# Kernel tuning notes

Hardware: AMD Instinct MI355X
Metric: run time of the kernel (lower is better)

The kernel has to match this reference:

```python
import jax, jax.numpy as jnp
import numpy as np

N = 100000      # nodes
DEG = 16        # in-degree per node -> E = 1.6M edges
F = 16          # data.x feature dim (19 total - 3 pos dims)
P = 3           # pos dim
H = 64          # hidden_dim
R = 8           # num_regions
C = 8           # num_classes


def _xavier(k, shp):
    lim = np.sqrt(6.0 / (shp[0] + shp[1])).astype(np.float32)
    return jax.random.uniform(k, shp, jnp.float32, -lim, lim)


def setup_inputs() -> dict:
    key = jax.random.key(0)
    ks = jax.random.split(key, 16)
    x = jax.random.normal(ks[0], (N, F), jnp.float32)
    pos = jax.random.uniform(ks[1], (N, P), jnp.float32)
    # every node is a target exactly DEG times so scatter-max is fully covered
    src = jax.random.randint(ks[2], (N * DEG,), 0, N, jnp.int32)
    tgt = jnp.repeat(jnp.arange(N, dtype=jnp.int32), DEG)
    edge_index = jnp.stack([src, tgt])
    # ---- CPU quotient-graph construction (mirrors sklearn KMeans + 3-NN) ----
    pos_np = np.asarray(pos)
    rng = np.random.RandomState(0)
    centers = pos_np[rng.choice(N, R, replace=False)].copy()
    for _ in range(10):  # Lloyd iterations
        d = ((pos_np[:, None, :] - centers[None, :, :]) ** 2).sum(-1)
        labels = d.argmin(1)
        for i in range(R):
            m = labels == i
            if m.any():
                centers[i] = pos_np[m].mean(0)
    cd = ((centers[:, None, :] - centers[None, :, :]) ** 2).sum(-1)
    nn_idx = np.argsort(cd, axis=1)[:, :3]
    conn = []
    for i in range(R):
        for j in nn_idx[i, 1:]:
            conn.append([i, j]); conn.append([j, i])
    quotient_edge_index = jnp.asarray(np.array(conn).T, jnp.int32)
    cluster_labels = jnp.asarray(labels, jnp.int32)
    # ---- parameters (xavier_uniform weights, zero bias) ----
    out = dict(x=x, pos=pos, edge_index=edge_index,
               cluster_labels=cluster_labels,
               quotient_edge_index=quotient_edge_index)
    in_dims = [2 * (F + P), 2 * H, 2 * H, 2 * H]
    for i in range(4):
        out[f"conv{i+1}_W1"] = _xavier(ks[3 + 2 * i], (in_dims[i], H))
        out[f"conv{i+1}_b1"] = jnp.zeros((H,), jnp.float32)
        out[f"conv{i+1}_W2"] = _xavier(ks[4 + 2 * i], (H, H))
        out[f"conv{i+1}_b2"] = jnp.zeros((H,), jnp.float32)
    out["lin_W"] = _xavier(ks[11], (H, C))
    out["lin_b"] = jnp.zeros((C,), jnp.float32)
    return out


def _edge_conv(x, edge_index, W1, b1, W2, b2, num_nodes):
    src, tgt = edge_index[0], edge_index[1]
    x_i = x[tgt]                         # [E, d] target (center)
    x_j = x[src]                         # [E, d] source (neighbor)
    m = jnp.concatenate([x_i, x_j - x_i], axis=1)   # [E, 2d]
    m = jax.nn.relu(m @ W1 + b1) @ W2 + b2          # [E, H]
    agg = jax.ops.segment_max(m, tgt, num_segments=num_nodes)
    # nodes with no incoming edges -> 0 (torch_scatter semantics)
    return jnp.where(jnp.isfinite(agg), agg, 0.0)


def reference(x, pos, edge_index, cluster_labels, quotient_edge_index,
              conv1_W1, conv1_b1, conv1_W2, conv1_b2,
              conv2_W1, conv2_b1, conv2_W2, conv2_b2,
              conv3_W1, conv3_b1, conv3_W2, conv3_b2,
              conv4_W1, conv4_b1, conv4_W2, conv4_b2,
              lin_W, lin_b):
    h = jnp.concatenate([x, pos], axis=1)                       # [N, 19]
    h = jax.nn.relu(_edge_conv(h, edge_index, conv1_W1, conv1_b1, conv1_W2, conv1_b2, N))
    h = jax.nn.relu(_edge_conv(h, edge_index, conv2_W1, conv2_b1, conv2_W2, conv2_b2, N))
    # quotient graph: per-region mean of node features
    sums = jax.ops.segment_sum(h, cluster_labels, num_segments=R)        # [R, H]
    cnt = jax.ops.segment_sum(jnp.ones((h.shape[0], 1), h.dtype), cluster_labels, num_segments=R)
    qx = jnp.where(cnt > 0, sums / jnp.maximum(cnt, 1.0), 0.0)           # [R, H]
    qx = jax.nn.relu(_edge_conv(qx, quotient_edge_index, conv3_W1, conv3_b1, conv3_W2, conv3_b2, R))
    qx = jax.nn.relu(_edge_conv(qx, quotient_edge_index, conv4_W1, conv4_b1, conv4_W2, conv4_b2, R))
    graph_emb = qx.sum(axis=0, keepdims=True)                    # global_add_pool -> [1, H]
    return graph_emb @ lin_W + lin_b                             # [1, C]
```

## Files before the change

kernel.cpp:

```cpp
#include <hip/hip_runtime.h>
#include <hip/hip_fp16.h>

typedef float fv4 __attribute__((ext_vector_type(4)));
using hf8   = __attribute__((ext_vector_type(8))) _Float16;
using f32x4 = __attribute__((ext_vector_type(4))) float;
using u32x4 = __attribute__((ext_vector_type(4))) unsigned;
using u32x2 = __attribute__((ext_vector_type(2))) unsigned;

#define HDIM 64
#define QBANKS 64

__device__ __forceinline__ unsigned short f16r(float f) {
    return __half_as_ushort(__float2half(f));
}
__device__ __forceinline__ float hs2f(unsigned short s) {
    return __half2float(__ushort_as_half(s));
}
__device__ __forceinline__ unsigned addrelu2(unsigned ua, unsigned va) {
    unsigned s, r;
    asm("v_pk_add_f16 %0, %1, %2" : "=v"(s) : "v"(ua), "v"(va));
    asm("v_pk_max_f16 %0, %1, 0" : "=v"(r) : "v"(s));
    return r;
}

__global__ void pre1_kernel(
    const float* __restrict__ x, const float* __restrict__ pos,
    const float* __restrict__ W1, const float* __restrict__ b1,
    unsigned short* __restrict__ U, unsigned short* __restrict__ V, int N,
    int mainBlocks,
    const float* __restrict__ W2a, const float* __restrict__ W2b,
    const float* __restrict__ W1c,
    unsigned short* __restrict__ hiA, unsigned short* __restrict__ loA,
    unsigned short* __restrict__ hiB, unsigned short* __restrict__ loB,
    unsigned short* __restrict__ wph, unsigned short* __restrict__ wpl,
    const int* __restrict__ labels, int* __restrict__ qcnt)
{
    if ((int)blockIdx.x >= mainBlocks) {
        int idx = (blockIdx.x - mainBlocks) * 256 + threadIdx.x;
        if (idx < 4096) {
            int j = idx >> 6, c = idx & 63;
            float w = W2a[idx];
            unsigned short h = f16r(w);
            unsigned short l = f16r(w - hs2f(h));
            hiA[c * 64 + j] = h; loA[c * 64 + j] = l;
            w = W2b[idx];
            h = f16r(w);
            l = f16r(w - hs2f(h));
            hiB[c * 64 + j] = h; loB[c * 64 + j] = l;
        }
        if (idx < 8192) {
            int d = idx & 63, cp = idx >> 6;
            float w = (cp < 64) ? (W1c[d * 64 + cp] - W1c[(d + 64) * 64 + cp])
                                : W1c[(d + 64) * 64 + (cp - 64)];
            unsigned short h = f16r(w);
            unsigned short l = f16r(w - hs2f(h));
            wph[cp * 64 + d] = h;
            wpl[cp * 64 + d] = l;
        }
        {
            __shared__ int lh[8];
            int loc[8] = {0, 0, 0, 0, 0, 0, 0, 0};
            for (int n = idx; n < N; n += 8192) {
                int l = labels[n];
#pragma unroll
                for (int r = 0; r < 8; ++r) loc[r] += (l == r) ? 1 : 0;
            }
            if (threadIdx.x < 8) lh[threadIdx.x] = 0;
            __syncthreads();
#pragma unroll
            for (int r = 0; r < 8; ++r) if (loc[r]) atomicAdd(&lh[r], loc[r]);
            __syncthreads();
            if (threadIdx.x < 8) atomicAdd(&qcnt[threadIdx.x], lh[threadIdx.x]);
        }
        return;
    }

    int lane = threadIdx.x & 63;
    int gw   = (blockIdx.x * blockDim.x + threadIdx.x) >> 6;
    int tw   = (mainBlocks * blockDim.x) >> 6;

    float wd[19], wb[19];
#pragma unroll
    for (int d = 0; d < 19; ++d) {
        float a = W1[d * HDIM + lane];
        float b = W1[(d + 19) * HDIM + lane];
        wd[d] = a - b;
        wb[d] = b;
    }
    float bb = b1[lane];

    for (int n0 = gw * 4; n0 < N; n0 += tw * 4) {
        fv4  xx[4][4];
        float p0[4], p1[4], p2[4];
#pragma unroll
        for (int k = 0; k < 4; ++k) {
#pragma unroll
            for (int d4 = 0; d4 < 4; ++d4)
                xx[k][d4] = *(const fv4*)&x[(size_t)(n0 + k) * 16 + 4 * d4];
            p0[k] = pos[(size_t)(n0 + k) * 3 + 0];
            p1[k] = pos[(size_t)(n0 + k) * 3 + 1];
            p2[k] = pos[(size_t)(n0 + k) * 3 + 2];
        }
#pragma unroll
        for (int k = 0; k < 4; ++k) {
            float su = 0.f, sv = 0.f;
#pragma unroll
            for (int d4 = 0; d4 < 4; ++d4)
#pragma unroll
                for (int q = 0; q < 4; ++q) {
                    su += xx[k][d4][q] * wd[4 * d4 + q];
                    sv += xx[k][d4][q] * wb[4 * d4 + q];
                }
            su += p0[k] * wd[16] + p1[k] * wd[17] + p2[k] * wd[18];
            sv += p0[k] * wb[16] + p1[k] * wb[17] + p2[k] * wb[18];
            U[(size_t)(n0 + k) * HDIM + lane] = f16r(su + bb);
            V[(size_t)(n0 + k) * HDIM + lane] = f16r(sv);
        }
    }
}

__global__ __launch_bounds__(256, 2) void pre_mfma_kernel(
    const unsigned short* __restrict__ h,
    const unsigned short* __restrict__ Whi,
    const unsigned short* __restrict__ Wlo,
    const float* __restrict__ b1,
    unsigned short* __restrict__ U, unsigned short* __restrict__ V, int nTiles)
{
    int lane = threadIdx.x & 63;
    int quad = lane >> 4;
    int m    = lane & 15;
    int gw   = (blockIdx.x * blockDim.x + threadIdx.x) >> 6;
    int tw   = (gridDim.x * blockDim.x) >> 6;

    hf8 Bh[8][2], Bl[8][2];
#pragma unroll
    for (int nt = 0; nt < 8; ++nt)
#pragma unroll
        for (int ks = 0; ks < 2; ++ks) {
            int off = (nt * 16 + m) * 64 + ks * 32 + quad * 8;
            Bh[nt][ks] = *(const hf8*)&Whi[off];
            Bl[nt][ks] = *(const hf8*)&Wlo[off];
        }
    float bias[16];
#pragma unroll
    for (int nt = 0; nt < 4; ++nt)
#pragma unroll
        for (int r = 0; r < 4; ++r)
            bias[nt * 4 + r] = b1[nt * 16 + quad * 4 + r];

    for (int t = gw; t < nTiles; t += tw) {
        int base = t * 16;
        hf8 A[2];
#pragma unroll
        for (int ks = 0; ks < 2; ++ks)
            A[ks] = *(const hf8*)&h[(size_t)(base + m) * HDIM + ks * 32 + quad * 8];

        f32x4 acc[8] = {{0,0,0,0},{0,0,0,0},{0,0,0,0},{0,0,0,0},
                        {0,0,0,0},{0,0,0,0},{0,0,0,0},{0,0,0,0}};
#pragma unroll
        for (int ks = 0; ks < 2; ++ks)
#pragma unroll
            for (int nt = 0; nt < 8; ++nt) {
                acc[nt] = __builtin_amdgcn_mfma_f32_16x16x32_f16(Bl[nt][ks], A[ks], acc[nt], 0, 0, 0);
                acc[nt] = __builtin_amdgcn_mfma_f32_16x16x32_f16(Bh[nt][ks], A[ks], acc[nt], 0, 0, 0);
            }

#pragma unroll
        for (int nt = 0; nt < 8; ++nt) {
            unsigned short* __restrict__ dst = (nt < 4) ? U : V;
            int c0 = (nt & 3) * 16 + quad * 4;
            float a0 = acc[nt][0] + ((nt < 4) ? bias[nt * 4 + 0] : 0.f);
            float a1 = acc[nt][1] + ((nt < 4) ? bias[nt * 4 + 1] : 0.f);
            float a2 = acc[nt][2] + ((nt < 4) ? bias[nt * 4 + 2] : 0.f);
            float a3 = acc[nt][3] + ((nt < 4) ? bias[nt * 4 + 3] : 0.f);
            u32x2 pk;
            pk[0] = (unsigned)f16r(a0) | ((unsigned)f16r(a1) << 16);
            pk[1] = (unsigned)f16r(a2) | ((unsigned)f16r(a3) << 16);
            *(u32x2*)&dst[(size_t)(base + m) * HDIM + c0] = pk;
        }
    }
}

#define FOLD_HALF(V0, V1, OFF)                                                     \
    _Pragma("unroll")                                                              \
    for (int mt = 0; mt < 4; ++mt) {                                               \
        int urow = wave * 8 + (OFF) + mt;                                          \
        u32x4 u0 = *(const u32x4*)((const char*)Ush + urow * 128 + quad * 16);     \
        u32x4 u1 = *(const u32x4*)((const char*)Ush + urow * 128 + 64 + quad * 16);\
        u32x4 a0, a1;                                                              \
        _Pragma("unroll")                                                          \
        for (int p = 0; p < 4; ++p) {                                              \
            a0[p] = addrelu2(u0[p], V0[mt][p]);                                    \
            a1[p] = addrelu2(u1[p], V1[mt][p]);                                    \
        }                                                                          \
        hf8 A0 = __builtin_bit_cast(hf8, a0);                                      \
        hf8 A1 = __builtin_bit_cast(hf8, a1);                                      \
        f32x4 acc[4] = {{0,0,0,0},{0,0,0,0},{0,0,0,0},{0,0,0,0}};                  \
        _Pragma("unroll")                                                          \
        for (int nt = 0; nt < 4; ++nt) {                                           \
            int bb  = nt * 2048 + m * 128 + quad * 16;                             \
            int bs0 = bb ^ ((m & 7) << 4);                                         \
            int bs1 = (bb + 64) ^ ((m & 7) << 4);                                  \
            hf8 Bh0 = *(const hf8*)((const char*)Wsh + bs0);                       \
            hf8 Bl0 = *(const hf8*)((const char*)Wsh + 8192 + bs0);                \
            hf8 Bh1 = *(const hf8*)((const char*)Wsh + bs1);                       \
            hf8 Bl1 = *(const hf8*)((const char*)Wsh + 8192 + bs1);                \
            acc[nt] = __builtin_amdgcn_mfma_f32_16x16x32_f16(A0, Bl0, acc[nt], 0, 0, 0); \
            acc[nt] = __builtin_amdgcn_mfma_f32_16x16x32_f16(A0, Bh0, acc[nt], 0, 0, 0); \
            acc[nt] = __builtin_amdgcn_mfma_f32_16x16x32_f16(A1, Bl1, acc[nt], 0, 0, 0); \
            acc[nt] = __builtin_amdgcn_mfma_f32_16x16x32_f16(A1, Bh1, acc[nt], 0, 0, 0); \
        }                                                                          \
        float mx[4];                                                               \
        _Pragma("unroll")                                                          \
        for (int nt = 0; nt < 4; ++nt)                                             \
            mx[nt] = fmaxf(fmaxf(acc[nt][0], acc[nt][1]), fmaxf(acc[nt][2], acc[nt][3])); \
        _Pragma("unroll")                                                          \
        for (int nt = 0; nt < 4; ++nt) {                                           \
            mx[nt] = fmaxf(mx[nt], __shfl_xor(mx[nt], 16));                        \
            mx[nt] = fmaxf(mx[nt], __shfl_xor(mx[nt], 32));                        \
        }                                                                          \
        float val = (quad == 0) ? mx[0] : (quad == 1) ? mx[1] : (quad == 2) ? mx[2] : mx[3]; \
        float hv = fmaxf(val + b2v, 0.f);                                          \
        if constexpr (POOL) {                                                      \
            int lbl = __shfl(labv, (OFF) + mt);                                    \
            _Pragma("unroll")                                                      \
            for (int r = 0; r < 8; ++r) pacc[r] += (lbl == r) ? hv : 0.f;          \
        } else {                                                                   \
            out[(size_t)(nb + (OFF) + mt) * HDIM + lane] = f16r(hv);               \
        }                                                                          \
    }

template<int POOL>
__global__ __launch_bounds__(256, 3) void edge_mfma_kernel(
    const unsigned short* __restrict__ U, const unsigned short* __restrict__ V,
    const int* __restrict__ src,
    const unsigned short* __restrict__ Whi, const unsigned short* __restrict__ Wlo,
    const float* __restrict__ b2, unsigned short* __restrict__ out,
    const int* __restrict__ labels, float* __restrict__ qsums)
{
    __shared__ __align__(16) unsigned short Wsh[8192];
    __shared__ __align__(16) unsigned short Ush[2048];

    int tid  = threadIdx.x;
    int wave = tid >> 6;
    int lane = tid & 63;
    int quad = lane >> 4;
    int m    = lane & 15;

    int nbB = blockIdx.x * 32;
    int nb  = nbB + wave * 8;

#pragma unroll
    for (int it = 0; it < 4; ++it) {
        int chunk = it * 256 + tid;
        int reg   = it >> 1;
        int b     = (chunk & 511) * 16;
        int bs    = b ^ (((b >> 7) & 7) << 4);
        const unsigned short* sp = reg ? Wlo : Whi;
        u32x4 d = *(const u32x4*)((const char*)sp + b);
        *(u32x4*)((char*)Wsh + reg * 8192 + bs) = d;
    }
    *(u32x4*)((char*)Ush + tid * 16) =
        *(const u32x4*)((const char*)(U + (size_t)nbB * HDIM) + tid * 16);

    int  srcA = src[(size_t)nb * 16 + lane];
    int  srcB = src[(size_t)(nb + 4) * 16 + lane];
    float b2v = b2[lane];
    float pacc[8] = {0, 0, 0, 0, 0, 0, 0, 0};
    int labv = 0;
    if (POOL && lane < 8) labv = labels[nb + lane];

    __syncthreads();

    u32x4 vA0[4], vA1[4], vB0[4], vB1[4];
#pragma unroll
    for (int mt = 0; mt < 4; ++mt) {
        int s_ = __shfl(srcA, mt * 16 + m);
        const u32x4* vp = (const u32x4*)(V + (size_t)s_ * HDIM + quad * 8);
        vA0[mt] = vp[0]; vA1[mt] = vp[4];
    }
#pragma unroll
    for (int mt = 0; mt < 4; ++mt) {
        int s_ = __shfl(srcB, mt * 16 + m);
        const u32x4* vp = (const u32x4*)(V + (size_t)s_ * HDIM + quad * 8);
        vB0[mt] = vp[0]; vB1[mt] = vp[4];
    }

    FOLD_HALF(vA0, vA1, 0)
    FOLD_HALF(vB0, vB1, 4)

    if constexpr (POOL) {
        float* Wf = (float*)Wsh;
        __syncthreads();
#pragma unroll
        for (int r = 0; r < 8; ++r) Wf[wave * 512 + r * 64 + lane] = pacc[r];
        __syncthreads();
        float* qs = qsums + (blockIdx.x & (QBANKS - 1)) * 512;
        for (int idx = tid; idx < 512; idx += 256) {
            float s = Wf[idx] + Wf[512 + idx] + Wf[1024 + idx] + Wf[1536 + idx];
            atomicAdd(&qs[idx], s);
        }
    }
}

#define EQ_MAX 64
__global__ __launch_bounds__(1024) void tail_kernel(
                            const float* __restrict__ qsums, const int* __restrict__ qcnt,
                            const int* __restrict__ qei, int Eq,
                            const float* __restrict__ W31, const float* __restrict__ b31,
                            const float* __restrict__ W32, const float* __restrict__ b32,
                            const float* __restrict__ W41, const float* __restrict__ b41,
                            const float* __restrict__ W42, const float* __restrict__ b42,
                            const float* __restrict__ linW, const float* __restrict__ linb,
                            float* __restrict__ out)
{
    __shared__ float qx[512], uu[512], vv[512];
    __shared__ float hr[EQ_MAX * 64], me[EQ_MAX * 64];
    __shared__ __align__(16) float W2s[64 * 64];
    __shared__ float ps[2048];
    __shared__ int   qes[EQ_MAX], qet[EQ_MAX];
    __shared__ float emb[64];

    int tid = threadIdx.x;
    if (Eq > EQ_MAX) Eq = EQ_MAX;

    if (tid < Eq) { qes[tid] = qei[tid]; qet[tid] = qei[Eq + tid]; }

    {
        int idx = tid & 511, half = tid >> 9;
        float s = 0.f;
#pragma unroll
        for (int bk = half * 32; bk < half * 32 + 32; ++bk)
            s += qsums[bk * 512 + idx];
        ps[tid] = s;
    }
    __syncthreads();
    if (tid < 512) {
        int r = tid >> 6;
        int cc = qcnt[r];
        float tot = ps[tid] + ps[512 + tid];
        qx[tid] = (cc > 0) ? tot / (float)cc : 0.f;
    }
    __syncthreads();

    for (int layer = 0; layer < 2; ++layer) {
        const float* W1p = layer ? W41 : W31;
        const float* b1p = layer ? b41 : b31;
        const float* W2p = layer ? W42 : W32;
        const float* b2p = layer ? b42 : b32;

        *(fv4*)&W2s[tid * 4] = *(const fv4*)&W2p[tid * 4];

        {
            int idx = tid & 511, half = tid >> 9;
            int t = idx >> 6, c = idx & 63;
            float su = 0.f, sv = 0.f;
#pragma unroll 8
            for (int d = half * 32; d < half * 32 + 32; ++d) {
                float hv = qx[t * 64 + d];
                float a = W1p[d * 64 + c];
                float b = W1p[(d + 64) * 64 + c];
                su += hv * (a - b);
                sv += hv * b;
            }
            ps[tid] = su;
            ps[1024 + tid] = sv;
        }
        __syncthreads();
        if (tid < 512) {
            int c = tid & 63;
            uu[tid] = ps[tid] + ps[512 + tid] + b1p[c];
            vv[tid] = ps[1024 + tid] + ps[1536 + tid];
        }
        __syncthreads();

        for (int idx = tid; idx < Eq * 64; idx += 1024) {
            int e = idx >> 6, c = idx & 63;
            hr[idx] = fmaxf(uu[qet[e] * 64 + c] + vv[qes[e] * 64 + c], 0.f);
        }
        __syncthreads();

        {
            int c = tid & 63, e0 = tid >> 6;
            for (int e = e0; e < Eq; e += 16) {
                float acc = 0.f;
#pragma unroll 8
                for (int j = 0; j < 64; ++j)
                    acc += hr[e * 64 + j] * W2s[j * 64 + c];
                me[e * 64 + c] = acc;
            }
        }
        __syncthreads();

        if (tid < 512) {
            int t = tid >> 6, c = tid & 63;
            float a = -INFINITY;
            for (int e = 0; e < Eq; ++e)
                if (qet[e] == t) a = fmaxf(a, me[e * 64 + c]);
            float vout = (a == -INFINITY) ? 0.f : (a + b2p[c]);
            qx[tid] = fmaxf(vout, 0.f);
        }
        __syncthreads();
    }

    if (tid < 64) {
        float s = 0.f;
        for (int r = 0; r < 8; ++r) s += qx[r * 64 + tid];
        emb[tid] = s;
    }
    __syncthreads();
    if (tid < 8) {
        float o = linb[tid];
        for (int c = 0; c < 64; ++c) o += emb[c] * linW[c * 8 + tid];
        out[tid] = o;
    }
}

extern "C" void kernel_launch(void* const* d_in, const int* in_sizes, int n_in,
                              void* d_out, int out_size, void* d_ws, size_t ws_size,
                              hipStream_t stream)
{
    const float* x    = (const float*)d_in[0];
    const float* pos  = (const float*)d_in[1];
    const int*   ei   = (const int*)d_in[2];
    const int*   lbl  = (const int*)d_in[3];
    const int*   qei  = (const int*)d_in[4];
    const float* W11 = (const float*)d_in[5];
    const float* b11 = (const float*)d_in[6];
    const float* W12 = (const float*)d_in[7];
    const float* b12 = (const float*)d_in[8];
    const float* W21 = (const float*)d_in[9];
    const float* b21 = (const float*)d_in[10];
    const float* W22 = (const float*)d_in[11];
    const float* b22 = (const float*)d_in[12];
    const float* W31 = (const float*)d_in[13];
    const float* b31 = (const float*)d_in[14];
    const float* W32 = (const float*)d_in[15];
    const float* b32 = (const float*)d_in[16];
    const float* W41 = (const float*)d_in[17];
    const float* b41 = (const float*)d_in[18];
    const float* W42 = (const float*)d_in[19];
    const float* b42 = (const float*)d_in[20];
    const float* linW = (const float*)d_in[21];
    const float* linb = (const float*)d_in[22];

    int N  = in_sizes[0] / 16;
    int Eq = in_sizes[4] / 2;
    const int* src = ei;

    size_t NH = (size_t)N * HDIM;
    unsigned short* hbf = (unsigned short*)d_ws;
    unsigned short* Ub  = hbf + NH;
    unsigned short* Vb  = Ub + NH;
    unsigned short* w2h1 = Vb + NH;
    unsigned short* w2l1 = w2h1 + 4096;
    unsigned short* w2h2 = w2l1 + 4096;
    unsigned short* w2l2 = w2h2 + 4096;
    unsigned short* wph  = w2l2 + 4096;
    unsigned short* wpl  = wph + 8192;
    float* qsums = (float*)(wpl + 8192);
    int*   qcnt  = (int*)(qsums + QBANKS * 512);

    (void)hipMemsetAsync(qsums, 0, QBANKS * 512 * sizeof(float) + 8 * sizeof(int), stream);

    int nTiles      = N / 16;
    int edgeBlocks  = N / 32;
    int mainBlocks  = 2048;

    pre1_kernel<<<mainBlocks + 32, 256, 0, stream>>>(
        x, pos, W11, b11, Ub, Vb, N, mainBlocks,
        W12, W22, W21, w2h1, w2l1, w2h2, w2l2, wph, wpl, lbl, qcnt);
    edge_mfma_kernel<0><<<edgeBlocks, 256, 0, stream>>>(
        Ub, Vb, src, w2h1, w2l1, b12, hbf, lbl, qsums);
    pre_mfma_kernel<<<1563, 256, 0, stream>>>(hbf, wph, wpl, b21, Ub, Vb, nTiles);
    edge_mfma_kernel<1><<<edgeBlocks, 256, 0, stream>>>(
        Ub, Vb, src, w2h2, w2l2, b22, hbf, lbl, qsums);
    tail_kernel<<<1, 1024, 0, stream>>>(qsums, qcnt, qei, Eq,
                                        W31, b31, W32, b32,
                                        W41, b41, W42, b42,
                                        linW, linb, (float*)d_out);
}
```

Before: 280.1 us.

## Fuse conv2 pre-projection into conv1 edge kernel via shared-memory tile

Conv1's edge kernel now writes its 32-row output tile into shared memory, skipping the global hbf store. It then runs the conv2 first-layer projection (U/V halves) with MFMA, writing U2/V2 directly. This removes the separate pre_mfma_kernel launch and the global round trip of the hidden features. It needs an extra N×64 workspace buffer, falls back to the old path if the workspace is too small, and reads projection weights straight from global memory per wave.

```diff
diff --git a/kernel.cpp b/kernel.cpp
--- a/kernel.cpp
+++ b/kernel.cpp
@@ -221,22 +221,28 @@
         }                                                                          \
         float val = (quad == 0) ? mx[0] : (quad == 1) ? mx[1] : (quad == 2) ? mx[2] : mx[3]; \
         float hv = fmaxf(val + b2v, 0.f);                                          \
-        if constexpr (POOL) {                                                      \
+        if constexpr (MODE == 1) {                                                 \
             int lbl = __shfl(labv, (OFF) + mt);                                    \
             _Pragma("unroll")                                                      \
             for (int r = 0; r < 8; ++r) pacc[r] += (lbl == r) ? hv : 0.f;          \
+        } else if constexpr (MODE == 2) {                                          \
+            int wbyte = urow * 128 + ((lane * 2) ^ ((urow & 7) << 4));             \
+            *(unsigned short*)((char*)Ush + wbyte) = f16r(hv);                     \
         } else {                                                                   \
             out[(size_t)(nb + (OFF) + mt) * HDIM + lane] = f16r(hv);               \
         }                                                                          \
     }
 
-template<int POOL>
+template<int MODE>
 __global__ __launch_bounds__(256, 3) void edge_mfma_kernel(
     const unsigned short* __restrict__ U, const unsigned short* __restrict__ V,
     const int* __restrict__ src,
     const unsigned short* __restrict__ Whi, const unsigned short* __restrict__ Wlo,
     const float* __restrict__ b2, unsigned short* __restrict__ out,
-    const int* __restrict__ labels, float* __restrict__ qsums)
+    const int* __restrict__ labels, float* __restrict__ qsums,
+    const unsigned short* __restrict__ Wp_hi, const unsigned short* __restrict__ Wp_lo,
+    const float* __restrict__ b1n,
+    unsigned short* __restrict__ U2, unsigned short* __restrict__ V2)
 {
     __shared__ __align__(16) unsigned short Wsh[8192];
     __shared__ __align__(16) unsigned short Ush[2048];
@@ -268,7 +274,7 @@
     float b2v = b2[lane];
     float pacc[8] = {0, 0, 0, 0, 0, 0, 0, 0};
     int labv = 0;
-    if (POOL && lane < 8) labv = labels[nb + lane];
+    if (MODE == 1 && lane < 8) labv = labels[nb + lane];
 
     __syncthreads();
 
@@ -289,7 +295,7 @@
     FOLD_HALF(vA0, vA1, 0)
     FOLD_HALF(vB0, vB1, 4)
 
-    if constexpr (POOL) {
+    if constexpr (MODE == 1) {
         float* Wf = (float*)Wsh;
         __syncthreads();
 #pragma unroll
@@ -299,6 +305,49 @@
         for (int idx = tid; idx < 512; idx += 256) {
             float s = Wf[idx] + Wf[512 + idx] + Wf[1024 + idx] + Wf[1536 + idx];
             atomicAdd(&qs[idx], s);
+        }
+    }
+
+    if constexpr (MODE == 2) {
+        __syncthreads();
+        int tile = wave >> 1;
+        int hh2  = wave & 1;
+        int base = nbB + tile * 16;
+        int rowA = tile * 16 + m;
+        int xr   = (rowA & 7) << 4;
+        hf8 A0f = *(const hf8*)((const char*)Ush + rowA * 128 + ((quad * 16) ^ xr));
+        hf8 A1f = *(const hf8*)((const char*)Ush + rowA * 128 + ((64 + quad * 16) ^ xr));
+
+        hf8 Wh_[4][2], Wl_[4][2];
+#pragma unroll
+        for (int j = 0; j < 4; ++j)
+#pragma unroll
+            for (int ks = 0; ks < 2; ++ks) {
+                int off = ((hh2 * 4 + j) * 16 + m) * 64 + ks * 32 + quad * 8;
+                Wh_[j][ks] = *(const hf8*)&Wp_hi[off];
+                Wl_[j][ks] = *(const hf8*)&Wp_lo[off];
+            }
+        f32x4 acc2[4] = {{0,0,0,0},{0,0,0,0},{0,0,0,0},{0,0,0,0}};
+#pragma unroll
+        for (int j = 0; j < 4; ++j) {
+            acc2[j] = __builtin_amdgcn_mfma_f32_16x16x32_f16(Wl_[j][0], A0f, acc2[j], 0, 0, 0);
+            acc2[j] = __builtin_amdgcn_mfma_f32_16x16x32_f16(Wh_[j][0], A0f, acc2[j], 0, 0, 0);
+            acc2[j] = __builtin_amdgcn_mfma_f32_16x16x32_f16(Wl_[j][1], A1f, acc2[j], 0, 0, 0);
+            acc2[j] = __builtin_amdgcn_mfma_f32_16x16x32_f16(Wh_[j][1], A1f, acc2[j], 0, 0, 0);
+        }
+        unsigned short* __restrict__ dst2 = hh2 ? V2 : U2;
+#pragma unroll
+        for (int j = 0; j < 4; ++j) {
+            int c0 = j * 16 + quad * 4;
+            float a0 = acc2[j][0], a1 = acc2[j][1], a2 = acc2[j][2], a3 = acc2[j][3];
+            if (hh2 == 0) {
+                a0 += b1n[c0 + 0]; a1 += b1n[c0 + 1];
+                a2 += b1n[c0 + 2]; a3 += b1n[c0 + 3];
+            }
+            u32x2 pk;
+            pk[0] = (unsigned)f16r(a0) | ((unsigned)f16r(a1) << 16);
+            pk[1] = (unsigned)f16r(a2) | ((unsigned)f16r(a3) << 16);
+            *(u32x2*)&dst2[(size_t)(base + m) * HDIM + c0] = pk;
         }
     }
 }
@@ -460,6 +509,11 @@
     unsigned short* wpl  = wph + 8192;
     float* qsums = (float*)(wpl + 8192);
     int*   qcnt  = (int*)(qsums + QBANKS * 512);
+    unsigned short* V2 = (unsigned short*)(qcnt + 8);
+
+    size_t needBytes = ((char*)(V2 + NH)) - ((char*)d_ws);
+    bool fused = ws_size >= needBytes;
+    unsigned short* U2 = hbf;
 
     (void)hipMemsetAsync(qsums, 0, QBANKS * 512 * sizeof(float) + 8 * sizeof(int), stream);
 
@@ -470,11 +524,23 @@
     pre1_kernel<<<mainBlocks + 32, 256, 0, stream>>>(
         x, pos, W11, b11, Ub, Vb, N, mainBlocks,
         W12, W22, W21, w2h1, w2l1, w2h2, w2l2, wph, wpl, lbl, qcnt);
-    edge_mfma_kernel<0><<<edgeBlocks, 256, 0, stream>>>(
-        Ub, Vb, src, w2h1, w2l1, b12, hbf, lbl, qsums);
-    pre_mfma_kernel<<<1563, 256, 0, stream>>>(hbf, wph, wpl, b21, Ub, Vb, nTiles);
-    edge_mfma_kernel<1><<<edgeBlocks, 256, 0, stream>>>(
-        Ub, Vb, src, w2h2, w2l2, b22, hbf, lbl, qsums);
+
+    if (fused) {
+        edge_mfma_kernel<2><<<edgeBlocks, 256, 0, stream>>>(
+            Ub, Vb, src, w2h1, w2l1, b12, nullptr, lbl, qsums,
+            wph, wpl, b21, U2, V2);
+        edge_mfma_kernel<1><<<edgeBlocks, 256, 0, stream>>>(
+            U2, V2, src, w2h2, w2l2, b22, nullptr, lbl, qsums,
+            nullptr, nullptr, nullptr, nullptr, nullptr);
+    } else {
+        edge_mfma_kernel<0><<<edgeBlocks, 256, 0, stream>>>(
+            Ub, Vb, src, w2h1, w2l1, b12, hbf, lbl, qsums,
+            nullptr, nullptr, nullptr, nullptr, nullptr);
+        pre_mfma_kernel<<<1563, 256, 0, stream>>>(hbf, wph, wpl, b21, Ub, Vb, nTiles);
+        edge_mfma_kernel<1><<<edgeBlocks, 256, 0, stream>>>(
+            Ub, Vb, src, w2h2, w2l2, b22, hbf, lbl, qsums,
+            nullptr, nullptr, nullptr, nullptr, nullptr);
+    }
     tail_kernel<<<1, 1024, 0, stream>>>(qsums, qcnt, qei, Eq,
                                         W31, b31, W32, b32,
                                         W41, b41, W42, b42,
```

Result: faster. 274.4 us, median of 2 (-2.0%).
